# Kernel tuning notes

Measured on AMD Instinct MI355X. Metric: run time of the kernel, lower is better.

Reference implementation:

```python
import jax, jax.numpy as jnp
import numpy as np

IN, H, B = 1024, 1024, 8192
EPS = 1e-5

def _ln(x, g, b):
    mu = jnp.mean(x, axis=-1, keepdims=True)
    var = jnp.mean(jnp.square(x - mu), axis=-1, keepdims=True)
    return (x - mu) * jax.lax.rsqrt(var + EPS) * g + b

def setup_inputs() -> dict:
    key = jax.random.key(0)
    ks = jax.random.split(key, 6)
    inp = {
        "input": jax.random.normal(ks[0], (B, IN), dtype=jnp.float32),
        "h_prev": jax.random.normal(ks[1], (B, H), dtype=jnp.float32),
        "c_prev": jax.random.normal(ks[2], (B, H), dtype=jnp.float32),
        # Linear(in, 4H, bias=False) weights, stored [out, in] like torch
        "w_i": jax.random.normal(ks[3], (4 * H, IN), dtype=jnp.float32) / np.sqrt(IN),
        "w_h": jax.random.normal(ks[4], (4 * H, H), dtype=jnp.float32) / np.sqrt(H),
    }
    for name in ("ln_i", "ln_h", "ln_g", "ln_o", "ln_c"):
        inp[name + "_g"] = jnp.ones((H,), dtype=jnp.float32)
        inp[name + "_b"] = jnp.zeros((H,), dtype=jnp.float32)
    return inp

def reference(input, h_prev, c_prev, w_i, w_h,
              ln_i_g, ln_i_b, ln_h_g, ln_h_b, ln_g_g, ln_g_b,
              ln_o_g, ln_o_b, ln_c_g, ln_c_b):
    gi = input @ w_i.T            # [B, 4H]
    gh = h_prev @ w_h.T           # [B, 4H]
    i_i, i_f, i_gc, i_o = jnp.split(gi, 4, axis=-1)
    h_i, h_f, h_g, h_o = jnp.split(gh, 4, axis=-1)
    i_g = jax.nn.sigmoid(_ln(i_i + h_i, ln_i_g, ln_i_b))
    f_g = jax.nn.sigmoid(_ln(i_f + h_f, ln_h_g, ln_h_b))
    # NOTE: faithful to source bug — uses sigmoided i_g (not chunk i_gc) here
    g_g = jnp.tanh(_ln(i_g + h_g, ln_g_g, ln_g_b))
    o_g = jax.nn.sigmoid(_ln(i_o + h_o, ln_o_g, ln_o_b))
    c_new = _ln(f_g * c_prev + i_g * g_g, ln_c_g, ln_c_b)
    h_new = o_g * jnp.tanh(c_new)
    return (h_new, c_new)
```

## Files before the change

kernel.cpp:

```cpp
#include <hip/hip_runtime.h>
#include <hip/hip_bf16.h>

#define BATCH 8192
#define HDIM  1024
#define KDIM  2048
#define NDIM  4096

__device__ inline unsigned short f2bf(float x) {
    unsigned int u = __float_as_uint(x);
    unsigned int r = (u + 0x7fffu + ((u >> 16) & 1u)) >> 16;
    return (unsigned short)r;
}
__device__ inline float bf2f(unsigned short u) {
    return __uint_as_float((unsigned int)u << 16);
}

typedef __attribute__((ext_vector_type(8))) unsigned short us8;

__global__ __launch_bounds__(256) void convert_kernel(
    const float* __restrict__ wi, const float* __restrict__ wh,
    const float* __restrict__ input, const float* __restrict__ h_prev,
    unsigned short* __restrict__ Wb, unsigned short* __restrict__ Xb)
{
    int idx = blockIdx.x * 256 + threadIdx.x;
    const int NW = NDIM * 256;
    float4 v0, v1;
    unsigned short* dst;
    if (idx < NW) {
        int n = idx >> 8;
        int k = (idx & 255) << 3;
        if (k < 1024) {
            if (n >= 2048 && n < 3072) {
                v0 = make_float4(0.f, 0.f, 0.f, 0.f);
                v1 = v0;
            } else {
                v0 = *(const float4*)(wi + (size_t)n * 1024 + k);
                v1 = *(const float4*)(wi + (size_t)n * 1024 + k + 4);
            }
        } else {
            v0 = *(const float4*)(wh + (size_t)n * 1024 + (k - 1024));
            v1 = *(const float4*)(wh + (size_t)n * 1024 + (k - 1024) + 4);
        }
        dst = Wb + (size_t)n * KDIM + k;
    } else {
        int j = idx - NW;
        int r = j >> 8;
        int k = (j & 255) << 3;
        if (k < 1024) {
            v0 = *(const float4*)(input + (size_t)r * 1024 + k);
            v1 = *(const float4*)(input + (size_t)r * 1024 + k + 4);
        } else {
            v0 = *(const float4*)(h_prev + (size_t)r * 1024 + (k - 1024));
            v1 = *(const float4*)(h_prev + (size_t)r * 1024 + (k - 1024) + 4);
        }
        dst = Xb + (size_t)r * KDIM + k;
    }
    us8 o;
    o[0] = f2bf(v0.x); o[1] = f2bf(v0.y); o[2] = f2bf(v0.z); o[3] = f2bf(v0.w);
    o[4] = f2bf(v1.x); o[5] = f2bf(v1.y); o[6] = f2bf(v1.z); o[7] = f2bf(v1.w);
    *(us8*)dst = o;
}

#define BM 256
#define BN 128
#define BK 64

typedef __attribute__((ext_vector_type(8))) short bf16x8;
typedef __attribute__((ext_vector_type(4))) float f32x4;

__global__ __launch_bounds__(512) void gemm_bt_kernel(
    const unsigned short* __restrict__ A,
    const unsigned short* __restrict__ Bw,
    unsigned short* __restrict__ G,
    int M)
{
    __shared__ unsigned short As[BM * BK];
    __shared__ unsigned short Bs[BN * BK];

    const int tid  = threadIdx.x;
    const int lane = tid & 63;
    const int wave = tid >> 6;

    const int bid = blockIdx.x;
    const int bm  = (bid >> 5) * BM;
    const int bn  = (bid & 31) * BN;

    f32x4 acc[4][4] = {};

    const int wm = (wave >> 1) * 64;
    const int wn = (wave & 1) * 64;

    const int srow = lane >> 3;
    const int c_sw = (lane & 7) ^ srow;

    int k0 = 0;
    if (bn >= 2048 && bn < 3072) k0 = 1024;

    for (; k0 < KDIM; k0 += BK) {
#pragma unroll
        for (int p = 0; p < 4; ++p) {
            const int rbase = wave * 32 + p * 8;
            const unsigned short* gA =
                A + (size_t)(bm + rbase + srow) * KDIM + k0 + c_sw * 8;
            __builtin_amdgcn_global_load_lds(
                (const __attribute__((address_space(1))) void*)gA,
                (__attribute__((address_space(3))) void*)&As[rbase * BK], 16, 0, 0);
        }
#pragma unroll
        for (int p = 0; p < 2; ++p) {
            const int rbase = wave * 16 + p * 8;
            const unsigned short* gB =
                Bw + (size_t)(bn + rbase + srow) * KDIM + k0 + c_sw * 8;
            __builtin_amdgcn_global_load_lds(
                (const __attribute__((address_space(1))) void*)gB,
                (__attribute__((address_space(3))) void*)&Bs[rbase * BK], 16, 0, 0);
        }
        __syncthreads();

#pragma unroll
        for (int kk = 0; kk < 2; ++kk) {
            bf16x8 af[4], bfr[4];
            const int cbase = kk * 4 + (lane >> 4);
#pragma unroll
            for (int i = 0; i < 4; ++i) {
                const int ra = wm + i * 16 + (lane & 15);
                af[i]  = *(const bf16x8*)&As[ra * BK + ((cbase ^ (ra & 7)) * 8)];
                const int rb = wn + i * 16 + (lane & 15);
                bfr[i] = *(const bf16x8*)&Bs[rb * BK + ((cbase ^ (rb & 7)) * 8)];
            }
#pragma unroll
            for (int i = 0; i < 4; ++i)
#pragma unroll
                for (int j = 0; j < 4; ++j)
                    acc[i][j] = __builtin_amdgcn_mfma_f32_16x16x32_bf16(
                        af[i], bfr[j], acc[i][j], 0, 0, 0);
        }
        __syncthreads();
    }

#pragma unroll
    for (int i = 0; i < 4; ++i) {
#pragma unroll
        for (int j = 0; j < 4; ++j) {
#pragma unroll
            for (int r = 0; r < 4; ++r) {
                int row = bm + wm + i * 16 + (lane >> 4) * 4 + r;
                int col = bn + wn + j * 16 + (lane & 15);
                G[(size_t)row * NDIM + col] = f2bf(acc[i][j][r]);
            }
        }
    }
}

__device__ inline float fast_rcp(float x) { return __builtin_amdgcn_rcpf(x); }
__device__ inline float sigmoid_f(float x) {
    return fast_rcp(1.f + __expf(-x));
}
__device__ inline float tanh_f(float x) {
    return 1.f - 2.f * fast_rcp(__expf(2.f * x) + 1.f);
}

__device__ inline void wstats(const float* x, float& mu, float& rs)
{
    float s = 0.f, q = 0.f;
#pragma unroll
    for (int e = 0; e < 16; ++e) { s += x[e]; q += x[e] * x[e]; }
#pragma unroll
    for (int o = 1; o < 64; o <<= 1) {
        s += __shfl_xor(s, o);
        q += __shfl_xor(q, o);
    }
    mu = s * (1.f / 1024.f);
    float var = q * (1.f / 1024.f) - mu * mu;
    rs = rsqrtf(var + 1e-5f);
}

#define LOADG16(dst, basep)                                            \
    _Pragma("unroll")                                                  \
    for (int j = 0; j < 2; ++j) {                                      \
        us8 t = *(const us8*)((basep) + j * 512 + cbase);              \
        _Pragma("unroll")                                              \
        for (int e = 0; e < 8; ++e) dst[j * 8 + e] = bf2f(t[e]);       \
    }

#define LOADF16(dst, basep)                                            \
    _Pragma("unroll")                                                  \
    for (int j = 0; j < 2; ++j) {                                      \
        float4 a = *(const float4*)((basep) + j * 512 + cbase);        \
        float4 b = *(const float4*)((basep) + j * 512 + cbase + 4);    \
        dst[j * 8 + 0] = a.x; dst[j * 8 + 1] = a.y;                    \
        dst[j * 8 + 2] = a.z; dst[j * 8 + 3] = a.w;                    \
        dst[j * 8 + 4] = b.x; dst[j * 8 + 5] = b.y;                    \
        dst[j * 8 + 6] = b.z; dst[j * 8 + 7] = b.w;                    \
    }

__global__ __launch_bounds__(256) void lstm_ew_kernel(
    const unsigned short* __restrict__ G,
    const float* __restrict__ c_prev,
    const float* __restrict__ p0g, const float* __restrict__ p0b,
    const float* __restrict__ p1g, const float* __restrict__ p1b,
    const float* __restrict__ p2g, const float* __restrict__ p2b,
    const float* __restrict__ p3g, const float* __restrict__ p3b,
    const float* __restrict__ p4g, const float* __restrict__ p4b,
    float* __restrict__ out_h, float* __restrict__ out_c,
    int row_base)
{
    const int lane  = threadIdx.x & 63;
    const int wave  = threadIdx.x >> 6;
    const int r     = blockIdx.x * 4 + wave;
    const int grow  = row_base + r;
    const int cbase = lane * 8;

    const unsigned short* Grow = G + (size_t)r * NDIM;

    float tmp[16], pg[16], pb[16];
    float ig[16], cm[16], og[16];
    float mu, rs;

    LOADG16(tmp, Grow);
    wstats(tmp, mu, rs);
    LOADF16(pg, p0g); LOADF16(pb, p0b);
#pragma unroll
    for (int e = 0; e < 16; ++e)
        ig[e] = sigmoid_f((tmp[e] - mu) * rs * pg[e] + pb[e]);

    LOADG16(tmp, Grow + 1024);
    wstats(tmp, mu, rs);
    LOADF16(pg, p1g); LOADF16(pb, p1b);
    LOADF16(cm, c_prev + (size_t)grow * HDIM);
#pragma unroll
    for (int e = 0; e < 16; ++e)
        cm[e] *= sigmoid_f((tmp[e] - mu) * rs * pg[e] + pb[e]);

    LOADG16(tmp, Grow + 2048);
#pragma unroll
    for (int e = 0; e < 16; ++e) tmp[e] += ig[e];
    wstats(tmp, mu, rs);
    LOADF16(pg, p2g); LOADF16(pb, p2b);
#pragma unroll
    for (int e = 0; e < 16; ++e)
        cm[e] += ig[e] * tanh_f((tmp[e] - mu) * rs * pg[e] + pb[e]);

    LOADG16(tmp, Grow + 3072);
    wstats(tmp, mu, rs);
    LOADF16(pg, p3g); LOADF16(pb, p3b);
#pragma unroll
    for (int e = 0; e < 16; ++e)
        og[e] = sigmoid_f((tmp[e] - mu) * rs * pg[e] + pb[e]);

    wstats(cm, mu, rs);
    LOADF16(pg, p4g); LOADF16(pb, p4b);
    float cn[16], hn[16];
#pragma unroll
    for (int e = 0; e < 16; ++e) {
        cn[e] = (cm[e] - mu) * rs * pg[e] + pb[e];
        hn[e] = og[e] * tanh_f(cn[e]);
    }

    float* oh = out_h + (size_t)grow * HDIM;
    float* oc = out_c + (size_t)grow * HDIM;
#pragma unroll
    for (int j = 0; j < 2; ++j) {
        *(float4*)(oh + j * 512 + cbase) =
            make_float4(hn[j*8+0], hn[j*8+1], hn[j*8+2], hn[j*8+3]);
        *(float4*)(oh + j * 512 + cbase + 4) =
            make_float4(hn[j*8+4], hn[j*8+5], hn[j*8+6], hn[j*8+7]);
        *(float4*)(oc + j * 512 + cbase) =
            make_float4(cn[j*8+0], cn[j*8+1], cn[j*8+2], cn[j*8+3]);
        *(float4*)(oc + j * 512 + cbase + 4) =
            make_float4(cn[j*8+4], cn[j*8+5], cn[j*8+6], cn[j*8+7]);
    }
}

extern "C" void kernel_launch(void* const* d_in, const int* in_sizes, int n_in,
                              void* d_out, int out_size, void* d_ws, size_t ws_size,
                              hipStream_t stream)
{
    const float* input  = (const float*)d_in[0];
    const float* h_prev = (const float*)d_in[1];
    const float* c_prev = (const float*)d_in[2];
    const float* w_i    = (const float*)d_in[3];
    const float* w_h    = (const float*)d_in[4];
    const float* lng[10];
    for (int i = 0; i < 10; ++i) lng[i] = (const float*)d_in[5 + i];

    unsigned short* Xb = (unsigned short*)d_ws;
    size_t xb_bytes = (size_t)BATCH * KDIM * 2;
    unsigned short* Wb = (unsigned short*)((char*)d_ws + xb_bytes);
    size_t wb_bytes = (size_t)NDIM * KDIM * 2;
    unsigned short* G = (unsigned short*)((char*)d_ws + xb_bytes + wb_bytes);

    convert_kernel<<<(NDIM * 256 + BATCH * 256) / 256, 256, 0, stream>>>(
        w_i, w_h, input, h_prev, Wb, Xb);

    float* out_h = (float*)d_out;
    float* out_c = out_h + (size_t)BATCH * HDIM;

    gemm_bt_kernel<<<(BATCH / BM) * (NDIM / BN), 512, 0, stream>>>(
        Xb, Wb, G, BATCH);
    lstm_ew_kernel<<<BATCH / 4, 256, 0, stream>>>(
        G, c_prev, lng[0], lng[1], lng[2], lng[3], lng[4],
        lng[5], lng[6], lng[7], lng[8], lng[9], out_h, out_c, 0);
}
```

Measured before the change: 334.3 us.

## Double-buffer GEMM with 256x256 tiles and phased load/MFMA interleave

After: 344.7 us. 1.03x slower.

```diff
diff --git a/kernel.cpp b/kernel.cpp
--- a/kernel.cpp
+++ b/kernel.cpp
@@ -62,11 +62,55 @@
 }
 
 #define BM 256
-#define BN 128
+#define BN 256
 #define BK 64
 
 typedef __attribute__((ext_vector_type(8))) short bf16x8;
 typedef __attribute__((ext_vector_type(4))) float f32x4;
+
+#define PHASE_BAR() { asm volatile("" ::: "memory"); \
+                      __builtin_amdgcn_s_barrier();  \
+                      asm volatile("" ::: "memory"); }
+
+#define STAGE_HALF_A(b, h, kt)                                                 \
+  { _Pragma("unroll") for (int p = 0; p < 2; ++p) {                            \
+      const int rbase = (wave >> 2) * 128 + (h) * 64 + (wave & 3) * 16 + p * 8;\
+      __builtin_amdgcn_global_load_lds(                                        \
+        (const __attribute__((address_space(1))) void*)(                       \
+            A + (size_t)(bm + rbase + srow) * KDIM + k0 + (kt) * BK + c_sw * 8),\
+        (__attribute__((address_space(3))) void*)&As[b][rbase * BK], 16, 0, 0);\
+  } }
+#define STAGE_HALF_B(b, h, kt)                                                 \
+  { _Pragma("unroll") for (int p = 0; p < 2; ++p) {                            \
+      const int rbase = (wave >> 1) * 64 + (h) * 32 + (wave & 1) * 16 + p * 8; \
+      __builtin_amdgcn_global_load_lds(                                        \
+        (const __attribute__((address_space(1))) void*)(                       \
+            Bw + (size_t)(bn + rbase + srow) * KDIM + k0 + (kt) * BK + c_sw * 8),\
+        (__attribute__((address_space(3))) void*)&Bs[b][rbase * BK], 16, 0, 0);\
+  } }
+
+#define READ_A4(buf, dst, mh)                                                  \
+  { _Pragma("unroll") for (int i = 0; i < 4; ++i)                              \
+    _Pragma("unroll") for (int kk = 0; kk < 2; ++kk) {                         \
+      const int ra = wm + (mh) * 64 + i * 16 + ln15;                           \
+      dst[i][kk] = *(const bf16x8*)                                            \
+          &As[buf][ra * BK + (((kk * 4 + l16) ^ (ra & 7)) * 8)]; } }
+#define READ_B2(buf, dst, nh)                                                  \
+  { _Pragma("unroll") for (int j = 0; j < 2; ++j)                              \
+    _Pragma("unroll") for (int kk = 0; kk < 2; ++kk) {                         \
+      const int rb = wn + (nh) * 32 + j * 16 + ln15;                           \
+      dst[j][kk] = *(const bf16x8*)                                            \
+          &Bs[buf][rb * BK + (((kk * 4 + l16) ^ (rb & 7)) * 8)]; } }
+
+#define MFMA_Q(mh, nh, av, bv)                                                 \
+  { __builtin_amdgcn_s_setprio(1);                                             \
+    _Pragma("unroll") for (int i = 0; i < 4; ++i)                              \
+    _Pragma("unroll") for (int j = 0; j < 2; ++j)                              \
+    _Pragma("unroll") for (int kk = 0; kk < 2; ++kk)                           \
+      acc[(mh) * 4 + i][(nh) * 2 + j] =                                        \
+          __builtin_amdgcn_mfma_f32_16x16x32_bf16(                             \
+              av[i][kk], bv[j][kk], acc[(mh) * 4 + i][(nh) * 2 + j], 0, 0, 0); \
+    __builtin_amdgcn_s_setprio(0); }
 
 __global__ __launch_bounds__(512) void gemm_bt_kernel(
     const unsigned short* __restrict__ A,
@@ -74,78 +118,81 @@
     unsigned short* __restrict__ G,
     int M)
 {
-    __shared__ unsigned short As[BM * BK];
-    __shared__ unsigned short Bs[BN * BK];
+    __shared__ unsigned short As[2][BM * BK];
+    __shared__ unsigned short Bs[2][BN * BK];
 
     const int tid  = threadIdx.x;
     const int lane = tid & 63;
     const int wave = tid >> 6;
 
     const int bid = blockIdx.x;
-    const int bm  = (bid >> 5) * BM;
-    const int bn  = (bid & 31) * BN;
-
-    f32x4 acc[4][4] = {};
-
-    const int wm = (wave >> 1) * 64;
-    const int wn = (wave & 1) * 64;
+    const int bm  = (bid >> 4) * BM;
+    const int bn  = (bid & 15) * BN;
+
+    const int wm = (wave >> 2) * 128;
+    const int wn = (wave & 3) * 64;
 
     const int srow = lane >> 3;
     const int c_sw = (lane & 7) ^ srow;
 
+    const int ln15 = lane & 15;
+    const int l16  = lane >> 4;
+
+    f32x4 acc[8][4] = {};
+
     int k0 = 0;
     if (bn >= 2048 && bn < 3072) k0 = 1024;
-
-    for (; k0 < KDIM; k0 += BK) {
-#pragma unroll
-        for (int p = 0; p < 4; ++p) {
-            const int rbase = wave * 32 + p * 8;
-            const unsigned short* gA =
-                A + (size_t)(bm + rbase + srow) * KDIM + k0 + c_sw * 8;
-            __builtin_amdgcn_global_load_lds(
-                (const __attribute__((address_space(1))) void*)gA,
-                (__attribute__((address_space(3))) void*)&As[rbase * BK], 16, 0, 0);
+    const int nt = (KDIM - k0) / BK;
+
+    STAGE_HALF_A(0, 0, 0); STAGE_HALF_B(0, 0, 0);
+    STAGE_HALF_A(0, 1, 0); STAGE_HALF_B(0, 1, 0);
+    STAGE_HALF_B(1, 0, 1); STAGE_HALF_A(1, 1, 1); STAGE_HALF_B(1, 1, 1);
+    asm volatile("s_waitcnt vmcnt(6)" ::: "memory");
+    PHASE_BAR();
+
+    for (int t = 0; t < nt; ++t) {
+        const int cur = t & 1;
+        const int nxt = cur ^ 1;
+        bf16x8 a0[4][2], a1[4][2], b0[2][2], b1[2][2];
+
+        READ_A4(cur, a0, 0); READ_B2(cur, b0, 0);
+        if (t + 1 < nt) STAGE_HALF_A(nxt, 0, t + 1);
+        PHASE_BAR();
+        MFMA_Q(0, 0, a0, b0);
+        PHASE_BAR();
+
+        READ_A4(cur, a1, 1);
+        if (t + 2 < nt) STAGE_HALF_B(cur, 0, t + 2);
+        PHASE_BAR();
+        MFMA_Q(1, 0, a1, b0);
+        PHASE_BAR();
+
+        READ_B2(cur, b1, 1);
+        if (t + 2 < nt) STAGE_HALF_A(cur, 1, t + 2);
+        PHASE_BAR();
+        MFMA_Q(1, 1, a1, b1);
+        PHASE_BAR();
+
+        READ_A4(cur, a0, 0);
+        if (t + 2 < nt) {
+            STAGE_HALF_B(cur, 1, t + 2);
+            asm volatile("s_waitcnt vmcnt(6)" ::: "memory");
+        } else if (t + 1 < nt) {
+            asm volatile("s_waitcnt vmcnt(0)" ::: "memory");
         }
-#pragma unroll
-        for (int p = 0; p < 2; ++p) {
-            const int rbase = wave * 16 + p * 8;
-            const unsigned short* gB =
-                Bw + (size_t)(bn + rbase + srow) * KDIM + k0 + c_sw * 8;
-            __builtin_amdgcn_global_load_lds(
-                (const __attribute__((address_space(1))) void*)gB,
-                (__attribute__((address_space(3))) void*)&Bs[rbase * BK], 16, 0, 0);
-        }
-        __syncthreads();
-
-#pragma unroll
-        for (int kk = 0; kk < 2; ++kk) {
-            bf16x8 af[4], bfr[4];
-            const int cbase = kk * 4 + (lane >> 4);
-#pragma unroll
-            for (int i = 0; i < 4; ++i) {
-                const int ra = wm + i * 16 + (lane & 15);
-                af[i]  = *(const bf16x8*)&As[ra * BK + ((cbase ^ (ra & 7)) * 8)];
-                const int rb = wn + i * 16 + (lane & 15);
-                bfr[i] = *(const bf16x8*)&Bs[rb * BK + ((cbase ^ (rb & 7)) * 8)];
-            }
-#pragma unroll
-            for (int i = 0; i < 4; ++i)
-#pragma unroll
-                for (int j = 0; j < 4; ++j)
-                    acc[i][j] = __builtin_amdgcn_mfma_f32_16x16x32_bf16(
-                        af[i], bfr[j], acc[i][j], 0, 0, 0);
-        }
-        __syncthreads();
-    }
-
-#pragma unroll
-    for (int i = 0; i < 4; ++i) {
+        PHASE_BAR();
+        MFMA_Q(0, 1, a0, b1);
+        PHASE_BAR();
+    }
+
+#pragma unroll
+    for (int i = 0; i < 8; ++i) {
 #pragma unroll
         for (int j = 0; j < 4; ++j) {
 #pragma unroll
             for (int r = 0; r < 4; ++r) {
-                int row = bm + wm + i * 16 + (lane >> 4) * 4 + r;
-                int col = bn + wn + j * 16 + (lane & 15);
+                int row = bm + wm + i * 16 + l16 * 4 + r;
+                int col = bn + wn + j * 16 + ln15;
                 G[(size_t)row * NDIM + col] = f2bf(acc[i][j][r]);
             }
         }
```
